# Kernel optimization log

Measured on AMD Instinct MI355X. Metric: run time of the kernel, lower is better.

The kernel has to match this reference:

```python
import jax, jax.numpy as jnp
import numpy as np

N_CODES = 4096
DIM = 1280
N_TOKENS = 32768


def _l2norm(v, axis=-1, eps=1e-12):
    return v / jnp.maximum(jnp.linalg.norm(v, axis=axis, keepdims=True), eps)


def setup_inputs() -> dict:
    key = jax.random.key(0)
    kx, ke = jax.random.split(key)
    # inputs are L2-normalized vectors per the module's docstring
    x = _l2norm(jax.random.normal(kx, (N_TOKENS, DIM), dtype=jnp.float32))
    # codebook init: uniform(-1/n_codes, 1/n_codes) then L2-normalized (as in __init__)
    embed = jax.random.uniform(ke, (N_CODES, DIM), dtype=jnp.float32,
                               minval=-1.0 / N_CODES, maxval=1.0 / N_CODES)
    embed = _l2norm(embed)
    return {"x": x, "embed": embed}


def reference(x, embed):
    x_sq = jnp.sum(x * x, axis=1, keepdims=True)            # (N, 1)
    e_sq = jnp.sum(embed * embed, axis=1)[None, :]          # (1, K)
    dist = -(x_sq - 2.0 * (x @ embed.T) + e_sq)             # (N, K)
    indices = jnp.argmax(dist, axis=-1)                     # (N,)
    quantized = embed[indices]                              # gather (N, D)
    commit_loss = jnp.mean((x - quantized) ** 2)
    # straight-through estimator
    quantized_ste = x + jax.lax.stop_gradient(quantized - x)
    return quantized_ste, indices, commit_loss
```

## Files before the change

### kernel.cpp

```cpp
#include <hip/hip_runtime.h>
#include <hip/hip_bf16.h>

typedef int i32x4 __attribute__((ext_vector_type(4)));

#define N_TOKENS 32768
#define N_CODES 4096
#define DIM 1280
#define NT 20
#define BUFSZ 32768

__device__ __forceinline__ void load_lds16(const void* g, void* l) {
    __builtin_amdgcn_global_load_lds(
        (const __attribute__((address_space(1))) unsigned int*)g,
        (__attribute__((address_space(3))) unsigned int*)l,
        16, 0, 0);
}

__global__ __launch_bounds__(256) void quantize_i8_kernel(
    const float* __restrict__ src, signed char* __restrict__ dst,
    float* __restrict__ scale, int nrows)
{
    int row = blockIdx.x * 4 + (threadIdx.x >> 6);
    if (row >= nrows) return;
    int lane = threadIdx.x & 63;
    const float4* s4 = (const float4*)(src + (size_t)row * DIM);
    float4 v[5];
    float amax = 0.f;
    #pragma unroll
    for (int j = 0; j < 5; ++j) {
        v[j] = s4[j * 64 + lane];
        amax = fmaxf(amax, fmaxf(fmaxf(fabsf(v[j].x), fabsf(v[j].y)),
                                 fmaxf(fabsf(v[j].z), fabsf(v[j].w))));
    }
    #pragma unroll
    for (int d = 1; d < 64; d <<= 1) amax = fmaxf(amax, __shfl_xor(amax, d));
    amax = fmaxf(amax, 1e-20f);
    float inv = 127.0f / amax;
    int* d4 = (int*)(dst + (size_t)row * DIM);
    #pragma unroll
    for (int j = 0; j < 5; ++j) {
        int q0 = (int)rintf(v[j].x * inv), q1 = (int)rintf(v[j].y * inv);
        int q2 = (int)rintf(v[j].z * inv), q3 = (int)rintf(v[j].w * inv);
        d4[j * 64 + lane] = (q0 & 0xFF) | ((q1 & 0xFF) << 8) |
                            ((q2 & 0xFF) << 16) | ((q3 & 0xFF) << 24);
    }
    if (lane == 0) scale[row] = amax * (1.0f / 127.0f);
}

__global__ __launch_bounds__(1024, 4) void gemm_argmax_kernel(
    const signed char* __restrict__ Xq, const signed char* __restrict__ Eq,
    const float* __restrict__ sx, const float* __restrict__ se,
    unsigned* __restrict__ pkeys)
{
    __shared__ __align__(16) char lds[4 * BUFSZ];

    int bid = blockIdx.x;
    int swz = (bid & 7) * 256 + (bid >> 3);
    int cb0 = swz >> 7, rb = swz & 127;
    int row0 = rb << 8, col0 = cb0 << 8;

    int tid = threadIdx.x;
    int wid = tid >> 6, lane = tid & 63;
    int wm = wid >> 2, wn = wid & 3;
    int lr = lane & 15, g = lane >> 4;

    int slot = (((lr & 1) << 2) + g) ^ ((lr >> 1) & 7);
    int aoff = ((wm << 5) + (lr >> 1)) * 128 + slot * 16;
    int boff = 16384 + ((wn << 5) + (lr >> 1)) * 128 + slot * 16;

    i32x4 acc[4][4] = {};

    auto STAGE = [&](int t) {
        int base = (t & 3) * BUFSZ;
        int k0 = t << 6;
        int f = tid;
        int rp = f >> 3, c = f & 7;
        int cp = c ^ (rp & 7);
        int gr = (rp << 1) + (cp >> 2);
        int kc = k0 + ((cp & 3) << 4);
        load_lds16(Xq + (size_t)(row0 + gr) * DIM + kc, lds + base + (f << 4));
        load_lds16(Eq + (size_t)(col0 + gr) * DIM + kc, lds + base + 16384 + (f << 4));
    };

    auto COMPUTE = [&](int t) {
        int base = (t & 3) * BUFSZ;
        const char* pA = lds + base + aoff;
        const char* pB = lds + base + boff;
        i32x4 a[4], b[4];
        #pragma unroll
        for (int m = 0; m < 4; ++m) a[m] = *(const i32x4*)(pA + (m << 10));
        #pragma unroll
        for (int n = 0; n < 4; ++n) b[n] = *(const i32x4*)(pB + (n << 10));
        __builtin_amdgcn_s_setprio(1);
        #pragma unroll
        for (int m = 0; m < 4; ++m)
            #pragma unroll
            for (int n = 0; n < 4; ++n)
                acc[m][n] = __builtin_amdgcn_mfma_i32_16x16x64_i8(
                    a[m], b[n], acc[m][n], 0, 0, 0);
        __builtin_amdgcn_s_setprio(0);
    };

    STAGE(0); STAGE(1); STAGE(2);
    asm volatile("s_waitcnt vmcnt(4)" ::: "memory");
    __builtin_amdgcn_s_barrier();
    __builtin_amdgcn_sched_barrier(0);

    for (int t = 0; t < NT - 3; ++t) {
        STAGE(t + 3);
        COMPUTE(t);
        asm volatile("s_waitcnt vmcnt(4)" ::: "memory");
        __builtin_amdgcn_s_barrier();
        __builtin_amdgcn_sched_barrier(0);
    }
    COMPUTE(NT - 3);
    asm volatile("s_waitcnt vmcnt(2)" ::: "memory");
    __builtin_amdgcn_s_barrier();
    __builtin_amdgcn_sched_barrier(0);
    COMPUTE(NT - 2);
    asm volatile("s_waitcnt vmcnt(0)" ::: "memory");
    __builtin_amdgcn_s_barrier();
    __builtin_amdgcn_sched_barrier(0);
    COMPUTE(NT - 1);
    __syncthreads();

    float se_l[4];
    #pragma unroll
    for (int n = 0; n < 4; ++n)
        se_l[n] = se[col0 + (wn << 6) + (n << 4) + lr];

    uint2* lk2 = (uint2*)lds;
    #pragma unroll
    for (int m = 0; m < 4; ++m) {
        #pragma unroll
        for (int r = 0; r < 4; ++r) {
            int row = (wm << 6) + (m << 4) + (g << 2) + r;
            float fx = sx[row0 + row];
            unsigned b1 = 0, b2 = 0;
            #pragma unroll
            for (int n = 0; n < 4; ++n) {
                float s = (float)acc[m][n][r] * (fx * se_l[n]);
                int cib = ((wn & 1) << 6) + (n << 4) + lr;
                unsigned u = __float_as_uint(s);
                u = (u & 0x80000000u) ? ~u : (u | 0x80000000u);
                unsigned key = (u & 0xFFFFFF80u) | (unsigned)(127 - cib);
                if (key > b1) { b2 = b1; b1 = key; }
                else if (key > b2) b2 = key;
            }
            #pragma unroll
            for (int d = 1; d < 16; d <<= 1) {
                unsigned o1 = __shfl_xor(b1, d), o2 = __shfl_xor(b2, d);
                if (o1 > b1) { b2 = (b1 > o2) ? b1 : o2; b1 = o1; }
                else if (o1 > b2) b2 = o1;
            }
            if (lr == 0) {
                uint2 v; v.x = b1; v.y = b2;
                lk2[(row << 2) + wn] = v;
            }
        }
    }
    __syncthreads();
    if (tid < 512) {
        int row = tid >> 1, h = tid & 1;
        uint2 p0 = lk2[(row << 2) + (h << 1)];
        uint2 p1 = lk2[(row << 2) + (h << 1) + 1];
        unsigned b1 = p0.x, b2 = p0.y;
        if (p1.x > b1) { b2 = (b1 > p1.y) ? b1 : p1.y; b1 = p1.x; }
        else if (p1.x > b2) b2 = p1.x;
        uint2 out; out.x = b1; out.y = b2;
        *(uint2*)&pkeys[((size_t)(row0 + row) << 6) + (((cb0 << 1) + h) << 1)] = out;
    }
}

__global__ __launch_bounds__(64) void refine_gather_kernel(
    const float* __restrict__ X, const float* __restrict__ E,
    const unsigned* __restrict__ pkeys, float* __restrict__ outq,
    float* __restrict__ outidx, float* __restrict__ sums)
{
    int token = blockIdx.x;
    int lane = threadIdx.x;
    unsigned k = pkeys[((size_t)token << 6) + lane];
    unsigned m = k & 0xFFFFFF80u;
    float s = __uint_as_float((m & 0x80000000u) ? (m & 0x7FFFFFFFu) : ~m);
    float smax = s;
    #pragma unroll
    for (int d = 1; d < 64; d <<= 1) smax = fmaxf(smax, __shfl_xor(smax, d));
    bool cand = s >= smax - 3e-3f;
    unsigned long long ball = __ballot(cand);

    const float4* x4 = (const float4*)(X + (size_t)token * DIM);
    float4 xv[5];
    #pragma unroll
    for (int j = 0; j < 5; ++j) xv[j] = x4[j * 64 + lane];

    double best_s = -1.0e300;
    int best_i = 0x7FFFFFFF;
    while (ball) {
        int src = __ffsll(ball) - 1;
        ball &= ball - 1;
        unsigned ck = __shfl(k, src);
        int cidx = ((src >> 1) << 7) + (127 - (int)(ck & 127u));
        const float4* e4 = (const float4*)(E + (size_t)cidx * DIM);
        double d = 0.0, ee = 0.0;
        #pragma unroll
        for (int j = 0; j < 5; ++j) {
            float4 ev = e4[j * 64 + lane];
            d += (double)xv[j].x * (double)ev.x + (double)xv[j].y * (double)ev.y
               + (double)xv[j].z * (double)ev.z + (double)xv[j].w * (double)ev.w;
            ee += (double)ev.x * (double)ev.x + (double)ev.y * (double)ev.y
                + (double)ev.z * (double)ev.z + (double)ev.w * (double)ev.w;
        }
        #pragma unroll
        for (int dd = 1; dd < 64; dd <<= 1) {
            d += __shfl_xor(d, dd);
            ee += __shfl_xor(ee, dd);
        }
        double sc = 2.0 * d - ee;
        if (sc > best_s || (sc == best_s && cidx < best_i)) { best_s = sc; best_i = cidx; }
    }

    const float4* e4 = (const float4*)(E + (size_t)best_i * DIM);
    float4* o4 = (float4*)(outq + (size_t)token * DIM);
    float local = 0.0f;
    #pragma unroll
    for (int j = 0; j < 5; ++j) {
        float4 q = e4[j * 64 + lane];
        o4[j * 64 + lane] = q;
        float dx = xv[j].x - q.x, dy = xv[j].y - q.y;
        float dz = xv[j].z - q.z, dw = xv[j].w - q.w;
        local += dx * dx + dy * dy + dz * dz + dw * dw;
    }
    #pragma unroll
    for (int d = 1; d < 64; d <<= 1) local += __shfl_xor(local, d);
    if (lane == 0) {
        sums[token] = local;
        outidx[token] = (float)best_i;
    }
}

__global__ __launch_bounds__(256) void loss_kernel(
    const float* __restrict__ sums, float* __restrict__ out_loss)
{
    __shared__ double red[256];
    int t = threadIdx.x;
    double s = 0.0;
    for (int i = t; i < N_TOKENS; i += 256) s += (double)sums[i];
    red[t] = s;
    __syncthreads();
    for (int off = 128; off > 0; off >>= 1) {
        if (t < off) red[t] += red[t + off];
        __syncthreads();
    }
    if (t == 0) out_loss[0] = (float)(red[0] / (double)((size_t)N_TOKENS * DIM));
}

extern "C" void kernel_launch(void* const* d_in, const int* in_sizes, int n_in,
                              void* d_out, int out_size, void* d_ws, size_t ws_size,
                              hipStream_t stream)
{
    const float* X = (const float*)d_in[0];
    const float* E = (const float*)d_in[1];

    float* outq = (float*)d_out;
    float* outidx = outq + (size_t)N_TOKENS * DIM;
    float* outloss = outidx + N_TOKENS;

    signed char* Xq = (signed char*)d_out;
    signed char* Eq = Xq + (size_t)N_TOKENS * DIM;
    float* sxs = (float*)(Eq + (size_t)N_CODES * DIM);
    float* ses = sxs + N_TOKENS;

    unsigned* pkeys = (unsigned*)d_ws;
    float* sums = (float*)((char*)d_ws + (size_t)N_TOKENS * 64 * sizeof(unsigned));

    quantize_i8_kernel<<<dim3(N_TOKENS / 4), dim3(256), 0, stream>>>(X, Xq, sxs, N_TOKENS);
    quantize_i8_kernel<<<dim3(N_CODES / 4), dim3(256), 0, stream>>>(E, Eq, ses, N_CODES);
    gemm_argmax_kernel<<<dim3(2048), dim3(1024), 0, stream>>>(Xq, Eq, sxs, ses, pkeys);
    refine_gather_kernel<<<dim3(N_TOKENS), dim3(64), 0, stream>>>(X, E, pkeys, outq, outidx, sums);
    loss_kernel<<<dim3(1), dim3(256), 0, stream>>>(sums, outloss);
}
```

Measured before the change: 380.6 us.

## Pre-swizzle X int8 into MFMA fragment layout and load A directly to registers

```diff
diff --git a/kernel.cpp b/kernel.cpp
--- a/kernel.cpp
+++ b/kernel.cpp
@@ -7,7 +7,6 @@
 #define N_CODES 4096
 #define DIM 1280
 #define NT 20
-#define BUFSZ 32768
 
 __device__ __forceinline__ void load_lds16(const void* g, void* l) {
     __builtin_amdgcn_global_load_lds(
@@ -16,6 +15,7 @@
         16, 0, 0);
 }
 
+template <bool FRAG>
 __global__ __launch_bounds__(256) void quantize_i8_kernel(
     const float* __restrict__ src, signed char* __restrict__ dst,
     float* __restrict__ scale, int nrows)
@@ -36,23 +36,30 @@
     for (int d = 1; d < 64; d <<= 1) amax = fmaxf(amax, __shfl_xor(amax, d));
     amax = fmaxf(amax, 1e-20f);
     float inv = 127.0f / amax;
-    int* d4 = (int*)(dst + (size_t)row * DIM);
     #pragma unroll
     for (int j = 0; j < 5; ++j) {
         int q0 = (int)rintf(v[j].x * inv), q1 = (int)rintf(v[j].y * inv);
         int q2 = (int)rintf(v[j].z * inv), q3 = (int)rintf(v[j].w * inv);
-        d4[j * 64 + lane] = (q0 & 0xFF) | ((q1 & 0xFF) << 8) |
-                            ((q2 & 0xFF) << 16) | ((q3 & 0xFF) << 24);
+        int w = (q0 & 0xFF) | ((q1 & 0xFF) << 8) |
+                ((q2 & 0xFF) << 16) | ((q3 & 0xFF) << 24);
+        if (FRAG) {
+            int c = (j * 64 + lane) << 2;
+            size_t dest = ((size_t)((row >> 8) * 20 + (c >> 6)) << 14)
+                        + (((row >> 4) & 15) << 10) + ((row & 15) << 6) + (c & 63);
+            *(int*)(dst + dest) = w;
+        } else {
+            ((int*)(dst + (size_t)row * DIM))[j * 64 + lane] = w;
+        }
     }
     if (lane == 0) scale[row] = amax * (1.0f / 127.0f);
 }
 
 __global__ __launch_bounds__(1024, 4) void gemm_argmax_kernel(
-    const signed char* __restrict__ Xq, const signed char* __restrict__ Eq,
+    const signed char* __restrict__ XqF, const signed char* __restrict__ Eq,
     const float* __restrict__ sx, const float* __restrict__ se,
     unsigned* __restrict__ pkeys)
 {
-    __shared__ __align__(16) char lds[4 * BUFSZ];
+    __shared__ __align__(16) char lds[4 * 16384];
 
     int bid = blockIdx.x;
     int swz = (bid & 7) * 256 + (bid >> 3);
@@ -65,30 +72,31 @@
     int lr = lane & 15, g = lane >> 4;
 
     int slot = (((lr & 1) << 2) + g) ^ ((lr >> 1) & 7);
-    int aoff = ((wm << 5) + (lr >> 1)) * 128 + slot * 16;
-    int boff = 16384 + ((wn << 5) + (lr >> 1)) * 128 + slot * 16;
+    int boff = ((wn << 5) + (lr >> 1)) * 128 + slot * 16;
+
+    const signed char* Aptr = XqF + (size_t)rb * (20 * 16384)
+                              + (wm << 12) + (lr << 6) + (g << 4);
 
     i32x4 acc[4][4] = {};
-
-    auto STAGE = [&](int t) {
-        int base = (t & 3) * BUFSZ;
-        int k0 = t << 6;
+    i32x4 a[4];
+
+    auto STAGE_B = [&](int t) {
+        int base = (t & 3) * 16384;
         int f = tid;
         int rp = f >> 3, c = f & 7;
         int cp = c ^ (rp & 7);
         int gr = (rp << 1) + (cp >> 2);
-        int kc = k0 + ((cp & 3) << 4);
-        load_lds16(Xq + (size_t)(row0 + gr) * DIM + kc, lds + base + (f << 4));
-        load_lds16(Eq + (size_t)(col0 + gr) * DIM + kc, lds + base + 16384 + (f << 4));
+        int kc = (t << 6) + ((cp & 3) << 4);
+        load_lds16(Eq + (size_t)(col0 + gr) * DIM + kc, lds + base + (f << 4));
     };
-
-    auto COMPUTE = [&](int t) {
-        int base = (t & 3) * BUFSZ;
-        const char* pA = lds + base + aoff;
-        const char* pB = lds + base + boff;
-        i32x4 a[4], b[4];
-        #pragma unroll
-        for (int m = 0; m < 4; ++m) a[m] = *(const i32x4*)(pA + (m << 10));
+    auto LOAD_A = [&](int t) {
+        const signed char* p = Aptr + (size_t)t * 16384;
+        #pragma unroll
+        for (int m = 0; m < 4; ++m) a[m] = *(const i32x4*)(p + (m << 10));
+    };
+    auto MFMA_T = [&](int t) {
+        const char* pB = lds + (t & 3) * 16384 + boff;
+        i32x4 b[4];
         #pragma unroll
         for (int n = 0; n < 4; ++n) b[n] = *(const i32x4*)(pB + (n << 10));
         __builtin_amdgcn_s_setprio(1);
@@ -101,27 +109,32 @@
         __builtin_amdgcn_s_setprio(0);
     };
 
-    STAGE(0); STAGE(1); STAGE(2);
-    asm volatile("s_waitcnt vmcnt(4)" ::: "memory");
-    __builtin_amdgcn_s_barrier();
-    __builtin_amdgcn_sched_barrier(0);
-
-    for (int t = 0; t < NT - 3; ++t) {
-        STAGE(t + 3);
-        COMPUTE(t);
-        asm volatile("s_waitcnt vmcnt(4)" ::: "memory");
-        __builtin_amdgcn_s_barrier();
-        __builtin_amdgcn_sched_barrier(0);
-    }
-    COMPUTE(NT - 3);
+    LOAD_A(0);
+    STAGE_B(0); STAGE_B(1); STAGE_B(2);
     asm volatile("s_waitcnt vmcnt(2)" ::: "memory");
     __builtin_amdgcn_s_barrier();
     __builtin_amdgcn_sched_barrier(0);
-    COMPUTE(NT - 2);
+
+    for (int t = 0; t < NT - 3; ++t) {
+        STAGE_B(t + 3);
+        asm volatile("s_waitcnt vmcnt(1)" ::: "memory");
+        MFMA_T(t);
+        LOAD_A(t + 1);
+        __builtin_amdgcn_s_barrier();
+        __builtin_amdgcn_sched_barrier(0);
+    }
+    asm volatile("s_waitcnt vmcnt(0)" ::: "memory");
+    MFMA_T(NT - 3);
+    LOAD_A(NT - 2);
     asm volatile("s_waitcnt vmcnt(0)" ::: "memory");
     __builtin_amdgcn_s_barrier();
     __builtin_amdgcn_sched_barrier(0);
-    COMPUTE(NT - 1);
+    MFMA_T(NT - 2);
+    LOAD_A(NT - 1);
+    asm volatile("s_waitcnt vmcnt(0)" ::: "memory");
+    __builtin_amdgcn_s_barrier();
+    __builtin_amdgcn_sched_barrier(0);
+    MFMA_T(NT - 1);
     __syncthreads();
 
     float se_l[4];
@@ -265,17 +278,17 @@
     float* outidx = outq + (size_t)N_TOKENS * DIM;
     float* outloss = outidx + N_TOKENS;
 
-    signed char* Xq = (signed char*)d_out;
-    signed char* Eq = Xq + (size_t)N_TOKENS * DIM;
+    signed char* XqF = (signed char*)d_out;
+    signed char* Eq = XqF + (size_t)N_TOKENS * DIM;
     float* sxs = (float*)(Eq + (size_t)N_CODES * DIM);
     float* ses = sxs + N_TOKENS;
 
     unsigned* pkeys = (unsigned*)d_ws;
     float* sums = (float*)((char*)d_ws + (size_t)N_TOKENS * 64 * sizeof(unsigned));
 
-    quantize_i8_kernel<<<dim3(N_TOKENS / 4), dim3(256), 0, stream>>>(X, Xq, sxs, N_TOKENS);
-    quantize_i8_kernel<<<dim3(N_CODES / 4), dim3(256), 0, stream>>>(E, Eq, ses, N_CODES);
-    gemm_argmax_kernel<<<dim3(2048), dim3(1024), 0, stream>>>(Xq, Eq, sxs, ses, pkeys);
+    quantize_i8_kernel<true><<<dim3(N_TOKENS / 4), dim3(256), 0, stream>>>(X, XqF, sxs, N_TOKENS);
+    quantize_i8_kernel<false><<<dim3(N_CODES / 4), dim3(256), 0, stream>>>(E, Eq, ses, N_CODES);
+    gemm_argmax_kernel<<<dim3(2048), dim3(1024), 0, stream>>>(XqF, Eq, sxs, ses, pkeys);
     refine_gather_kernel<<<dim3(N_TOKENS), dim3(64), 0, stream>>>(X, E, pkeys, outq, outidx, sums);
     loss_kernel<<<dim3(1), dim3(256), 0, stream>>>(sums, outloss);
 }
```

Result: slower. 449.9 us (+18.2%).

## Shrink GEMM tile to 128x256 with 512 threads, triple-buffer, merge quantize launches

Applied to the files above, without the earlier changes.

```diff
diff --git a/kernel.cpp b/kernel.cpp
--- a/kernel.cpp
+++ b/kernel.cpp
@@ -7,7 +7,8 @@
 #define N_CODES 4096
 #define DIM 1280
 #define NT 20
-#define BUFSZ 32768
+#define BUFSZ 24576
+#define NBUF 3
 
 __device__ __forceinline__ void load_lds16(const void* g, void* l) {
     __builtin_amdgcn_global_load_lds(
@@ -17,13 +18,23 @@
 }
 
 __global__ __launch_bounds__(256) void quantize_i8_kernel(
-    const float* __restrict__ src, signed char* __restrict__ dst,
-    float* __restrict__ scale, int nrows)
+    const float* __restrict__ X, const float* __restrict__ E,
+    signed char* __restrict__ Xq, signed char* __restrict__ Eq,
+    float* __restrict__ sxs, float* __restrict__ ses)
 {
     int row = blockIdx.x * 4 + (threadIdx.x >> 6);
-    if (row >= nrows) return;
+    const float* src;
+    signed char* dst;
+    float* scale;
+    if (row < N_TOKENS) {
+        src = X + (size_t)row * DIM; dst = Xq + (size_t)row * DIM; scale = sxs + row;
+    } else {
+        int r = row - N_TOKENS;
+        if (r >= N_CODES) return;
+        src = E + (size_t)r * DIM; dst = Eq + (size_t)r * DIM; scale = ses + r;
+    }
     int lane = threadIdx.x & 63;
-    const float4* s4 = (const float4*)(src + (size_t)row * DIM);
+    const float4* s4 = (const float4*)src;
     float4 v[5];
     float amax = 0.f;
     #pragma unroll
@@ -36,7 +47,7 @@
     for (int d = 1; d < 64; d <<= 1) amax = fmaxf(amax, __shfl_xor(amax, d));
     amax = fmaxf(amax, 1e-20f);
     float inv = 127.0f / amax;
-    int* d4 = (int*)(dst + (size_t)row * DIM);
+    int* d4 = (int*)dst;
     #pragma unroll
     for (int j = 0; j < 5; ++j) {
         int q0 = (int)rintf(v[j].x * inv), q1 = (int)rintf(v[j].y * inv);
@@ -44,20 +55,20 @@
         d4[j * 64 + lane] = (q0 & 0xFF) | ((q1 & 0xFF) << 8) |
                             ((q2 & 0xFF) << 16) | ((q3 & 0xFF) << 24);
     }
-    if (lane == 0) scale[row] = amax * (1.0f / 127.0f);
-}
-
-__global__ __launch_bounds__(1024, 4) void gemm_argmax_kernel(
+    if (lane == 0) *scale = amax * (1.0f / 127.0f);
+}
+
+__global__ __launch_bounds__(512, 4) void gemm_argmax_kernel(
     const signed char* __restrict__ Xq, const signed char* __restrict__ Eq,
     const float* __restrict__ sx, const float* __restrict__ se,
     unsigned* __restrict__ pkeys)
 {
-    __shared__ __align__(16) char lds[4 * BUFSZ];
+    __shared__ __align__(16) char lds[NBUF * BUFSZ];
 
     int bid = blockIdx.x;
-    int swz = (bid & 7) * 256 + (bid >> 3);
-    int cb0 = swz >> 7, rb = swz & 127;
-    int row0 = rb << 8, col0 = cb0 << 8;
+    int swz = (bid & 7) * 512 + (bid >> 3);
+    int cb = swz >> 8, rb = swz & 255;
+    int row0 = rb << 7, col0 = cb << 8;
 
     int tid = threadIdx.x;
     int wid = tid >> 6, lane = tid & 63;
@@ -66,24 +77,33 @@
 
     int slot = (((lr & 1) << 2) + g) ^ ((lr >> 1) & 7);
     int aoff = ((wm << 5) + (lr >> 1)) * 128 + slot * 16;
-    int boff = 16384 + ((wn << 5) + (lr >> 1)) * 128 + slot * 16;
+    int boff = 8192 + ((wn << 5) + (lr >> 1)) * 128 + slot * 16;
 
     i32x4 acc[4][4] = {};
 
     auto STAGE = [&](int t) {
-        int base = (t & 3) * BUFSZ;
+        int base = (t % NBUF) * BUFSZ;
         int k0 = t << 6;
-        int f = tid;
-        int rp = f >> 3, c = f & 7;
-        int cp = c ^ (rp & 7);
-        int gr = (rp << 1) + (cp >> 2);
-        int kc = k0 + ((cp & 3) << 4);
-        load_lds16(Xq + (size_t)(row0 + gr) * DIM + kc, lds + base + (f << 4));
-        load_lds16(Eq + (size_t)(col0 + gr) * DIM + kc, lds + base + 16384 + (f << 4));
+        {
+            int rp = tid >> 3, c = tid & 7;
+            int cp = c ^ (rp & 7);
+            int gr = (rp << 1) + (cp >> 2);
+            int kc = k0 + ((cp & 3) << 4);
+            load_lds16(Xq + (size_t)(row0 + gr) * DIM + kc, lds + base + (tid << 4));
+        }
+        #pragma unroll
+        for (int i = 0; i < 2; ++i) {
+            int f = tid + (i << 9);
+            int rp = f >> 3, c = f & 7;
+            int cp = c ^ (rp & 7);
+            int gr = (rp << 1) + (cp >> 2);
+            int kc = k0 + ((cp & 3) << 4);
+            load_lds16(Eq + (size_t)(col0 + gr) * DIM + kc, lds + base + 8192 + (f << 4));
+        }
     };
 
     auto COMPUTE = [&](int t) {
-        int base = (t & 3) * BUFSZ;
+        int base = (t % NBUF) * BUFSZ;
         const char* pA = lds + base + aoff;
         const char* pB = lds + base + boff;
         i32x4 a[4], b[4];
@@ -101,22 +121,18 @@
         __builtin_amdgcn_s_setprio(0);
     };
 
-    STAGE(0); STAGE(1); STAGE(2);
-    asm volatile("s_waitcnt vmcnt(4)" ::: "memory");
+    STAGE(0); STAGE(1);
+    asm volatile("s_waitcnt vmcnt(3)" ::: "memory");
     __builtin_amdgcn_s_barrier();
     __builtin_amdgcn_sched_barrier(0);
 
-    for (int t = 0; t < NT - 3; ++t) {
-        STAGE(t + 3);
+    for (int t = 0; t < NT - 2; ++t) {
+        STAGE(t + 2);
         COMPUTE(t);
-        asm volatile("s_waitcnt vmcnt(4)" ::: "memory");
+        asm volatile("s_waitcnt vmcnt(3)" ::: "memory");
         __builtin_amdgcn_s_barrier();
         __builtin_amdgcn_sched_barrier(0);
     }
-    COMPUTE(NT - 3);
-    asm volatile("s_waitcnt vmcnt(2)" ::: "memory");
-    __builtin_amdgcn_s_barrier();
-    __builtin_amdgcn_sched_barrier(0);
     COMPUTE(NT - 2);
     asm volatile("s_waitcnt vmcnt(0)" ::: "memory");
     __builtin_amdgcn_s_barrier();
@@ -160,7 +176,7 @@
         }
     }
     __syncthreads();
-    if (tid < 512) {
+    if (tid < 256) {
         int row = tid >> 1, h = tid & 1;
         uint2 p0 = lk2[(row << 2) + (h << 1)];
         uint2 p1 = lk2[(row << 2) + (h << 1) + 1];
@@ -168,7 +184,7 @@
         if (p1.x > b1) { b2 = (b1 > p1.y) ? b1 : p1.y; b1 = p1.x; }
         else if (p1.x > b2) b2 = p1.x;
         uint2 out; out.x = b1; out.y = b2;
-        *(uint2*)&pkeys[((size_t)(row0 + row) << 6) + (((cb0 << 1) + h) << 1)] = out;
+        *(uint2*)&pkeys[((size_t)(row0 + row) << 6) + (((cb << 1) + h) << 1)] = out;
     }
 }
 
@@ -273,9 +289,9 @@
     unsigned* pkeys = (unsigned*)d_ws;
     float* sums = (float*)((char*)d_ws + (size_t)N_TOKENS * 64 * sizeof(unsigned));
 
-    quantize_i8_kernel<<<dim3(N_TOKENS / 4), dim3(256), 0, stream>>>(X, Xq, sxs, N_TOKENS);
-    quantize_i8_kernel<<<dim3(N_CODES / 4), dim3(256), 0, stream>>>(E, Eq, ses, N_CODES);
-    gemm_argmax_kernel<<<dim3(2048), dim3(1024), 0, stream>>>(Xq, Eq, sxs, ses, pkeys);
+    quantize_i8_kernel<<<dim3((N_TOKENS + N_CODES) / 4), dim3(256), 0, stream>>>(
+        X, E, Xq, Eq, sxs, ses);
+    gemm_argmax_kernel<<<dim3(4096), dim3(512), 0, stream>>>(Xq, Eq, sxs, ses, pkeys);
     refine_gather_kernel<<<dim3(N_TOKENS), dim3(64), 0, stream>>>(X, E, pkeys, outq, outidx, sums);
     loss_kernel<<<dim3(1), dim3(256), 0, stream>>>(sums, outloss);
 }
```

Measured after the change: 380.5 us. About the same (-0.0%).
